# Kernel optimization log

Measured on AMD Instinct MI355X. Metric: run time of the kernel, lower is better.

## Reference

```python
import jax, jax.numpy as jnp
import numpy as np

B, L, D, DK, T = 8192, 64, 512, 64, 128
WIDE_IN = 2 * T + T * T  # 16640


def setup_inputs() -> dict:
    key = jax.random.key(0)
    ks = jax.random.split(key, 24)
    s = 0.02
    inp = {
        "mashup_tags": jax.random.uniform(ks[0], (B, T), jnp.float32),
        "target_api_tags": jax.random.uniform(ks[1], (B, T), jnp.float32),
        "cross_product_tag": jax.random.uniform(ks[2], (B, T * T), jnp.float32),
        "encoded_api_context": jax.random.normal(ks[3], (B, L, D), jnp.float32),
        "candidate_api_description_feature": jax.random.normal(ks[4], (B, D), jnp.float32),
        "mashup_description_feature": jax.random.normal(ks[5], (B, D), jnp.float32),
        "context_len": jax.random.randint(ks[6], (B,), 0, L + 1, jnp.int64 if jax.config.jax_enable_x64 else jnp.int32),
        # attention projections (torch Linear weight layout: [out, in], no bias)
        "W_K": s * jax.random.normal(ks[7], (DK, D), jnp.float32),
        "W_Q": s * jax.random.normal(ks[8], (DK, D), jnp.float32),
        # wide head
        "wide_w": s * jax.random.normal(ks[9], (1, WIDE_IN), jnp.float32),
        "wide_b": jnp.zeros((1,), jnp.float32),
        # deep MLP 1536->512->256->128->1
        "d1_w": s * jax.random.normal(ks[10], (512, 3 * D), jnp.float32),
        "d1_b": jnp.zeros((512,), jnp.float32),
        "d2_w": s * jax.random.normal(ks[11], (256, 512), jnp.float32),
        "d2_b": jnp.zeros((256,), jnp.float32),
        "d3_w": s * jax.random.normal(ks[12], (128, 256), jnp.float32),
        "d3_b": jnp.zeros((128,), jnp.float32),
        "d4_w": s * jax.random.normal(ks[13], (1, 128), jnp.float32),
        "d4_b": jnp.zeros((1,), jnp.float32),
        "wide_weight": jnp.ones((1,), jnp.float32),
        "deep_weight": jnp.ones((1,), jnp.float32),
        "bias": jnp.zeros((1,), jnp.float32),
    }
    return inp


def reference(mashup_tags, target_api_tags, cross_product_tag,
              encoded_api_context, candidate_api_description_feature,
              mashup_description_feature, context_len,
              W_K, W_Q, wide_w, wide_b,
              d1_w, d1_b, d2_w, d2_b, d3_w, d3_b, d4_w, d4_b,
              wide_weight, deep_weight, bias):
    # ---- wide branch ----
    wide_in = jnp.concatenate([mashup_tags, target_api_tags, cross_product_tag], axis=1)
    wide_out = jax.nn.sigmoid(wide_in @ wide_w.T + wide_b)  # (B,1)

    # ---- ragged attention (vectorized masked softmax replaces the Python batch loop) ----
    K = jnp.einsum("bld,kd->blk", encoded_api_context, W_K)          # (B,L,dk)
    Q = candidate_api_description_feature @ W_Q.T                     # (B,dk)
    scores = jnp.einsum("blk,bk->bl", K, Q)                           # (B,L)
    mask = jnp.arange(scores.shape[1])[None, :] < context_len[:, None]
    m = jnp.max(jnp.where(mask, scores, -1e30), axis=-1, keepdims=True)
    e = jnp.where(mask, jnp.exp(scores - m), 0.0)
    denom = jnp.sum(e, axis=-1, keepdims=True)
    probs = e / jnp.maximum(denom, 1e-30)  # rows with length==0 -> all zeros (matches torch zeros fallback)
    api_context = jnp.einsum("bl,bld->bd", probs, encoded_api_context)  # (B,512)

    # ---- deep branch ----
    deep_in = jnp.concatenate([mashup_description_feature, api_context,
                               candidate_api_description_feature], axis=1)  # (B,1536)
    h = jax.nn.relu(deep_in @ d1_w.T + d1_b)
    h = jax.nn.relu(h @ d2_w.T + d2_b)
    h = jax.nn.relu(h @ d3_w.T + d3_b)
    deep_out = h @ d4_w.T + d4_b  # (B,1)

    out = wide_weight * wide_out + deep_weight * deep_out + bias
    return jax.nn.sigmoid(out)
```

## Files before the change

### kernel.cpp

```cpp
#include <hip/hip_runtime.h>

#define Bsz 8192
#define Lctx 64
#define Ddim 512
#define DK 64
#define Ttag 128
#define RQT 4

using f32x4 = __attribute__((ext_vector_type(4))) float;
using bf16x8 = __attribute__((ext_vector_type(8))) short;

__device__ __forceinline__ float wave_sum(float v) {
#pragma unroll
    for (int m = 32; m > 0; m >>= 1) v += __shfl_xor(v, m, 64);
    return v;
}

__device__ __forceinline__ float dot4(float4 a, float4 b) {
    return a.x * b.x + a.y * b.y + a.z * b.z + a.w * b.w;
}

__device__ __forceinline__ unsigned f2bf(float f) {
    unsigned int u = __float_as_uint(f);
    u = u + 0x7fffu + ((u >> 16) & 1u);
    return u >> 16;
}
__device__ __forceinline__ unsigned pack2(float a, float b) {
    return f2bf(a) | (f2bf(b) << 16);
}
__device__ __forceinline__ float bf2f(unsigned short u) { return __uint_as_float((unsigned)u << 16); }

__global__ __launch_bounds__(256) void k_f2bf3(
    const float* __restrict__ s1, unsigned short* __restrict__ d1,
    const float* __restrict__ s2, unsigned short* __restrict__ d2,
    const float* __restrict__ s3, unsigned short* __restrict__ d3)
{
    int i = blockIdx.x * 256 + threadIdx.x;
    const float* s;
    unsigned short* d;
    if (i < 196608)      { s = s1; d = d1; }
    else if (i < 229376) { i -= 196608; s = s2; d = d2; }
    else if (i < 237568) { i -= 229376; s = s3; d = d3; }
    else return;
    const float4 v = ((const float4*)s)[i];
    uint2 w;
    w.x = pack2(v.x, v.y);
    w.y = pack2(v.z, v.w);
    *(uint2*)&d[(size_t)i * 4] = w;
}

__global__ __launch_bounds__(256) void k_qtilde(
    const float* __restrict__ C, const float* __restrict__ WQ,
    const float* __restrict__ WK, float* __restrict__ qt)
{
    const int lane = threadIdx.x & 63;
    const int gw = blockIdx.x * 4 + (threadIdx.x >> 6);
    const int b0 = gw * RQT;

    float4 c0[RQT], c1[RQT];
#pragma unroll
    for (int r = 0; r < RQT; ++r) {
        const float4* row = (const float4*)(C + (size_t)(b0 + r) * Ddim);
        c0[r] = row[lane];
        c1[r] = row[64 + lane];
    }
    float tv[RQT];
#pragma unroll
    for (int r = 0; r < RQT; ++r) tv[r] = 0.f;
    for (int k = 0; k < DK; ++k) {
        const float4* wrow = (const float4*)(WQ + (size_t)k * Ddim);
        const float4 w0 = wrow[lane];
        const float4 w1 = wrow[64 + lane];
#pragma unroll
        for (int r = 0; r < RQT; ++r) {
            float p = dot4(c0[r], w0) + dot4(c1[r], w1);
            p = wave_sum(p);
            if (lane == k) tv[r] = p;
        }
    }
    float4 a0[RQT], a1[RQT];
#pragma unroll
    for (int r = 0; r < RQT; ++r) {
        a0[r] = make_float4(0.f, 0.f, 0.f, 0.f);
        a1[r] = make_float4(0.f, 0.f, 0.f, 0.f);
    }
    for (int k = 0; k < DK; ++k) {
        const float4* wrow = (const float4*)(WK + (size_t)k * Ddim);
        const float4 w0 = wrow[lane];
        const float4 w1 = wrow[64 + lane];
#pragma unroll
        for (int r = 0; r < RQT; ++r) {
            const float tk = __shfl(tv[r], k, 64);
            a0[r].x += tk * w0.x; a0[r].y += tk * w0.y;
            a0[r].z += tk * w0.z; a0[r].w += tk * w0.w;
            a1[r].x += tk * w1.x; a1[r].y += tk * w1.y;
            a1[r].z += tk * w1.z; a1[r].w += tk * w1.w;
        }
    }
#pragma unroll
    for (int r = 0; r < RQT; ++r) {
        float4* orow = (float4*)(qt + (size_t)(b0 + r) * Ddim);
        orow[lane] = a0[r];
        orow[64 + lane] = a1[r];
    }
}

__global__ __launch_bounds__(256, 4) void k_attn_wide(
    const float* __restrict__ X, const float* __restrict__ qt,
    const int* __restrict__ clen, const float* __restrict__ mdesc,
    const float* __restrict__ cand,
    const float* __restrict__ mt, const float* __restrict__ tt,
    const float* __restrict__ cp, const float* __restrict__ ww,
    const float* __restrict__ wb,
    unsigned short* __restrict__ din, float* __restrict__ wl)
{
    const int tid = threadIdx.x;
    const int wave = tid >> 6, lane = tid & 63;
    const int b = blockIdx.x * 4 + wave;
    const int len = clen[b];

    const float4* qrow = (const float4*)(qt + (size_t)b * Ddim);
    const float4 q0 = qrow[lane];
    const float4 q1 = qrow[64 + lane];
    const float4* xb = (const float4*)(X + (size_t)b * Lctx * Ddim);

    float4 y0 = make_float4(0.f, 0.f, 0.f, 0.f);
    float4 y1 = make_float4(0.f, 0.f, 0.f, 0.f);
    float M = -1e30f, D = 0.f;

    const int nch = (len + 7) >> 3;
    for (int c = 0; c < nch; ++c) {
        const int base = c * 8;
        const int nr = min(8, len - base);
        float4 t0[8], t1[8];
#pragma unroll
        for (int r = 0; r < 8; ++r) {
            const int l = base + min(r, nr - 1);
            t0[r] = xb[l * 128 + lane];
            t1[r] = xb[l * 128 + 64 + lane];
        }
        float sc[8];
#pragma unroll
        for (int r = 0; r < 8; ++r)
            sc[r] = dot4(t0[r], q0) + dot4(t1[r], q1);
#pragma unroll
        for (int r = 0; r < 8; ++r) sc[r] = wave_sum(sc[r]);

        float pmax = -1e30f;
#pragma unroll
        for (int r = 0; r < 8; ++r)
            if (r < nr) pmax = fmaxf(pmax, sc[r]);
        const float Mn = fmaxf(M, pmax);
        const float scale = __expf(M - Mn);
        D *= scale;
        y0.x *= scale; y0.y *= scale; y0.z *= scale; y0.w *= scale;
        y1.x *= scale; y1.y *= scale; y1.z *= scale; y1.w *= scale;
#pragma unroll
        for (int r = 0; r < 8; ++r) {
            if (r < nr) {
                const float e = __expf(sc[r] - Mn);
                D += e;
                y0.x += e * t0[r].x; y0.y += e * t0[r].y;
                y0.z += e * t0[r].z; y0.w += e * t0[r].w;
                y1.x += e * t1[r].x; y1.y += e * t1[r].y;
                y1.z += e * t1[r].z; y1.w += e * t1[r].w;
            }
        }
        M = Mn;
    }

    float wacc;
    {
        const float2 a  = ((const float2*)(mt + (size_t)b * Ttag))[lane];
        const float2 wA = ((const float2*)ww)[lane];
        const float2 t  = ((const float2*)(tt + (size_t)b * Ttag))[lane];
        const float2 wB = ((const float2*)(ww + Ttag))[lane];
        wacc = a.x * wA.x + a.y * wA.y + t.x * wB.x + t.y * wB.y;
    }
    {
        const float4* cp4 = (const float4*)(cp + (size_t)b * (Ttag * Ttag));
        const float4* ww4 = (const float4*)(ww + 2 * Ttag);
        float wa = 0.f, wbk = 0.f;
#pragma unroll 8
        for (int i = 0; i < 64; i += 2) {
            wa  += dot4(cp4[i * 64 + lane],       ww4[i * 64 + lane]);
            wbk += dot4(cp4[(i + 1) * 64 + lane], ww4[(i + 1) * 64 + lane]);
        }
        wacc += wa + wbk;
    }
    wacc = wave_sum(wacc);
    if (lane == 0) wl[b] = wacc + wb[0];

    unsigned short* dr = din + (size_t)b * 1536;
    const float rden = 1.f / fmaxf(D, 1e-30f);
    {
        uint2 w;
        w.x = pack2(y0.x * rden, y0.y * rden);
        w.y = pack2(y0.z * rden, y0.w * rden);
        *(uint2*)&dr[512 + 4 * lane] = w;
        w.x = pack2(y1.x * rden, y1.y * rden);
        w.y = pack2(y1.z * rden, y1.w * rden);
        *(uint2*)&dr[512 + 256 + 4 * lane] = w;
    }
    {
        const float4* md = (const float4*)(mdesc + (size_t)b * Ddim);
        const float4 m0 = md[lane], m1 = md[64 + lane];
        uint2 w;
        w.x = pack2(m0.x, m0.y); w.y = pack2(m0.z, m0.w);
        *(uint2*)&dr[4 * lane] = w;
        w.x = pack2(m1.x, m1.y); w.y = pack2(m1.z, m1.w);
        *(uint2*)&dr[256 + 4 * lane] = w;
    }
    {
        const float4* cd = (const float4*)(cand + (size_t)b * Ddim);
        const float4 c0 = cd[lane], c1 = cd[64 + lane];
        uint2 w;
        w.x = pack2(c0.x, c0.y); w.y = pack2(c0.z, c0.w);
        *(uint2*)&dr[1024 + 4 * lane] = w;
        w.x = pack2(c1.x, c1.y); w.y = pack2(c1.z, c1.w);
        *(uint2*)&dr[1024 + 256 + 4 * lane] = w;
    }
}

__global__ __launch_bounds__(256) void k_gemm_bf16(
    const unsigned short* __restrict__ A, const unsigned short* __restrict__ W,
    const float* __restrict__ bias, unsigned short* __restrict__ C,
    const int K, const int N, const int relu)
{
    __shared__ unsigned short As[128][72];
    __shared__ unsigned short Bs[128][72];
    const int tid = threadIdx.x;
    const int wave = tid >> 6, lane = tid & 63;
    const int wm = wave >> 1, wn = wave & 1;
    const size_t m0 = (size_t)blockIdx.x * 128;
    const size_t n0 = (size_t)blockIdx.y * 128;

    f32x4 acc[4][4];
#pragma unroll
    for (int i = 0; i < 4; ++i)
#pragma unroll
        for (int j = 0; j < 4; ++j) acc[i][j] = (f32x4){0.f, 0.f, 0.f, 0.f};

    uint4 pa[4], pb[4];
    auto loadA = [&](int k0) {
#pragma unroll
        for (int j = 0; j < 4; ++j) {
            const int i = tid + j * 256;
            const int row = i >> 3, c8 = (i & 7) * 8;
            pa[j] = *(const uint4*)(A + (m0 + row) * (size_t)K + k0 + c8);
        }
    };
    auto loadB = [&](int k0) {
#pragma unroll
        for (int j = 0; j < 4; ++j) {
            const int i = tid + j * 256;
            const int row = i >> 3, c8 = (i & 7) * 8;
            pb[j] = *(const uint4*)(W + (n0 + row) * (size_t)K + k0 + c8);
        }
    };

    loadA(0);
    loadB(0);
    for (int k0 = 0; k0 < K; k0 += 64) {
        __syncthreads();
#pragma unroll
        for (int j = 0; j < 4; ++j) {
            const int i = tid + j * 256;
            const int row = i >> 3, c8 = (i & 7) * 8;
            *(uint4*)&As[row][c8] = pa[j];
            *(uint4*)&Bs[row][c8] = pb[j];
        }
        __syncthreads();
        if (k0 + 64 < K) { loadA(k0 + 64); loadB(k0 + 64); }
#pragma unroll
        for (int kk = 0; kk < 2; ++kk) {
            const int krow = kk * 32 + (lane >> 4) * 8;
            bf16x8 af[4], bfr[4];
#pragma unroll
            for (int mm = 0; mm < 4; ++mm)
                af[mm] = *(const bf16x8*)&As[wm * 64 + mm * 16 + (lane & 15)][krow];
#pragma unroll
            for (int nn = 0; nn < 4; ++nn)
                bfr[nn] = *(const bf16x8*)&Bs[wn * 64 + nn * 16 + (lane & 15)][krow];
#pragma unroll
            for (int mm = 0; mm < 4; ++mm)
#pragma unroll
                for (int nn = 0; nn < 4; ++nn)
                    acc[mm][nn] = __builtin_amdgcn_mfma_f32_16x16x32_bf16(
                        af[mm], bfr[nn], acc[mm][nn], 0, 0, 0);
        }
    }

#pragma unroll
    for (int nn = 0; nn < 4; ++nn) {
        const int col = (int)n0 + wn * 64 + nn * 16 + (lane & 15);
        const float bv = bias[col];
#pragma unroll
        for (int mm = 0; mm < 4; ++mm) {
#pragma unroll
            for (int r = 0; r < 4; ++r) {
                const size_t row = m0 + wm * 64 + mm * 16 + (lane >> 4) * 4 + r;
                float v = acc[mm][nn][r] + bv;
                if (relu) v = fmaxf(v, 0.f);
                C[row * N + col] = (unsigned short)f2bf(v);
            }
        }
    }
}

__global__ __launch_bounds__(256) void k_final(
    const unsigned short* __restrict__ h3, const float* __restrict__ d4w,
    const float* __restrict__ d4b, const float* __restrict__ wl,
    const float* __restrict__ wwt, const float* __restrict__ dwt,
    const float* __restrict__ bs, float* __restrict__ out)
{
    const int lane = threadIdx.x & 63;
    const int b = blockIdx.x * 4 + (threadIdx.x >> 6);
    const unsigned short* hr = h3 + (size_t)b * 128;
    float v = bf2f(hr[lane]) * d4w[lane] + bf2f(hr[64 + lane]) * d4w[64 + lane];
    v = wave_sum(v);
    if (lane == 0) {
        const float deep = v + d4b[0];
        const float wo = 1.f / (1.f + __expf(-wl[b]));
        const float z = wwt[0] * wo + dwt[0] * deep + bs[0];
        out[b] = 1.f / (1.f + __expf(-z));
    }
}

extern "C" void kernel_launch(void* const* d_in, const int* in_sizes, int n_in,
                              void* d_out, int out_size, void* d_ws, size_t ws_size,
                              hipStream_t stream)
{
    const float* mt    = (const float*)d_in[0];
    const float* tt    = (const float*)d_in[1];
    const float* cp    = (const float*)d_in[2];
    const float* X     = (const float*)d_in[3];
    const float* cand  = (const float*)d_in[4];
    const float* mdesc = (const float*)d_in[5];
    const int*   clen  = (const int*)d_in[6];
    const float* WK    = (const float*)d_in[7];
    const float* WQ    = (const float*)d_in[8];
    const float* ww    = (const float*)d_in[9];
    const float* wb    = (const float*)d_in[10];
    const float* d1w   = (const float*)d_in[11];
    const float* d1b   = (const float*)d_in[12];
    const float* d2w   = (const float*)d_in[13];
    const float* d2b   = (const float*)d_in[14];
    const float* d3w   = (const float*)d_in[15];
    const float* d3b   = (const float*)d_in[16];
    const float* d4w   = (const float*)d_in[17];
    const float* d4b   = (const float*)d_in[18];
    const float* wwt   = (const float*)d_in[19];
    const float* dwt   = (const float*)d_in[20];
    const float* bs    = (const float*)d_in[21];
    float* out = (float*)d_out;

    char* w = (char*)d_ws;
    unsigned short* din = (unsigned short*)w;            w += (size_t)Bsz * 1536 * 2;
    float* qt           = (float*)w;                     w += (size_t)Bsz * 512 * 4;
    unsigned short* h1  = (unsigned short*)w;            w += (size_t)Bsz * 512 * 2;
    unsigned short* h2  = (unsigned short*)w;            w += (size_t)Bsz * 256 * 2;
    unsigned short* h3  = (unsigned short*)w;            w += (size_t)Bsz * 128 * 2;
    float* wl           = (float*)w;                     w += (size_t)Bsz * 4;
    unsigned short* w1b = (unsigned short*)w;            w += (size_t)512 * 1536 * 2;
    unsigned short* w2b = (unsigned short*)w;            w += (size_t)256 * 512 * 2;
    unsigned short* w3b = (unsigned short*)w;            w += (size_t)128 * 256 * 2;

    hipLaunchKernelGGL(k_f2bf3, dim3(928), dim3(256), 0, stream,
                       d1w, w1b, d2w, w2b, d3w, w3b);
    hipLaunchKernelGGL(k_qtilde, dim3(Bsz / (RQT * 4)), dim3(256), 0, stream,
                       cand, WQ, WK, qt);
    hipLaunchKernelGGL(k_attn_wide, dim3(Bsz / 4), dim3(256), 0, stream,
                       X, qt, clen, mdesc, cand, mt, tt, cp, ww, wb, din, wl);
    hipLaunchKernelGGL(k_gemm_bf16, dim3(64, 4), dim3(256), 0, stream,
                       din, w1b, d1b, h1, 1536, 512, 1);
    hipLaunchKernelGGL(k_gemm_bf16, dim3(64, 2), dim3(256), 0, stream,
                       h1, w2b, d2b, h2, 512, 256, 1);
    hipLaunchKernelGGL(k_gemm_bf16, dim3(64, 1), dim3(256), 0, stream,
                       h2, w3b, d3b, h3, 256, 128, 1);
    hipLaunchKernelGGL(k_final, dim3(Bsz / 4), dim3(256), 0, stream,
                       h3, d4w, d4b, wl, wwt, dwt, bs, out);
}
```

Measured before the change: 438.5 us.

## Split wide head into per-row kernel and use narrower GEMM tiles

Moves the wide-branch dot product out of the attention kernel into a separate kernel with one 256-thread block per batch row. The attention chunk size drops from 8 to 4 context rows, and the bf16 GEMM is templated on N-tile width, using 64-wide tiles to double the grid size for the MLP layers. The goal is more memory-level parallelism and better CU occupancy. The cost is an extra launch, less load batching in attention, and more A-tile reloads in the GEMM.

Result: no change. 440.7 us (+0.5%).

```diff
diff --git a/kernel.cpp b/kernel.cpp
--- a/kernel.cpp
+++ b/kernel.cpp
@@ -105,14 +105,10 @@
     }
 }
 
-__global__ __launch_bounds__(256, 4) void k_attn_wide(
+__global__ __launch_bounds__(256, 4) void k_attn(
     const float* __restrict__ X, const float* __restrict__ qt,
     const int* __restrict__ clen, const float* __restrict__ mdesc,
-    const float* __restrict__ cand,
-    const float* __restrict__ mt, const float* __restrict__ tt,
-    const float* __restrict__ cp, const float* __restrict__ ww,
-    const float* __restrict__ wb,
-    unsigned short* __restrict__ din, float* __restrict__ wl)
+    const float* __restrict__ cand, unsigned short* __restrict__ din)
 {
     const int tid = threadIdx.x;
     const int wave = tid >> 6, lane = tid & 63;
@@ -128,27 +124,27 @@
     float4 y1 = make_float4(0.f, 0.f, 0.f, 0.f);
     float M = -1e30f, D = 0.f;
 
-    const int nch = (len + 7) >> 3;
+    const int nch = (len + 3) >> 2;
     for (int c = 0; c < nch; ++c) {
-        const int base = c * 8;
-        const int nr = min(8, len - base);
-        float4 t0[8], t1[8];
-#pragma unroll
-        for (int r = 0; r < 8; ++r) {
+        const int base = c * 4;
+        const int nr = min(4, len - base);
+        float4 t0[4], t1[4];
+#pragma unroll
+        for (int r = 0; r < 4; ++r) {
             const int l = base + min(r, nr - 1);
             t0[r] = xb[l * 128 + lane];
             t1[r] = xb[l * 128 + 64 + lane];
         }
-        float sc[8];
-#pragma unroll
-        for (int r = 0; r < 8; ++r)
+        float sc[4];
+#pragma unroll
+        for (int r = 0; r < 4; ++r)
             sc[r] = dot4(t0[r], q0) + dot4(t1[r], q1);
 #pragma unroll
-        for (int r = 0; r < 8; ++r) sc[r] = wave_sum(sc[r]);
+        for (int r = 0; r < 4; ++r) sc[r] = wave_sum(sc[r]);
 
         float pmax = -1e30f;
 #pragma unroll
-        for (int r = 0; r < 8; ++r)
+        for (int r = 0; r < 4; ++r)
             if (r < nr) pmax = fmaxf(pmax, sc[r]);
         const float Mn = fmaxf(M, pmax);
         const float scale = __expf(M - Mn);
@@ -156,7 +152,7 @@
         y0.x *= scale; y0.y *= scale; y0.z *= scale; y0.w *= scale;
         y1.x *= scale; y1.y *= scale; y1.z *= scale; y1.w *= scale;
 #pragma unroll
-        for (int r = 0; r < 8; ++r) {
+        for (int r = 0; r < 4; ++r) {
             if (r < nr) {
                 const float e = __expf(sc[r] - Mn);
                 D += e;
@@ -168,28 +164,6 @@
         }
         M = Mn;
     }
-
-    float wacc;
-    {
-        const float2 a  = ((const float2*)(mt + (size_t)b * Ttag))[lane];
-        const float2 wA = ((const float2*)ww)[lane];
-        const float2 t  = ((const float2*)(tt + (size_t)b * Ttag))[lane];
-        const float2 wB = ((const float2*)(ww + Ttag))[lane];
-        wacc = a.x * wA.x + a.y * wA.y + t.x * wB.x + t.y * wB.y;
-    }
-    {
-        const float4* cp4 = (const float4*)(cp + (size_t)b * (Ttag * Ttag));
-        const float4* ww4 = (const float4*)(ww + 2 * Ttag);
-        float wa = 0.f, wbk = 0.f;
-#pragma unroll 8
-        for (int i = 0; i < 64; i += 2) {
-            wa  += dot4(cp4[i * 64 + lane],       ww4[i * 64 + lane]);
-            wbk += dot4(cp4[(i + 1) * 64 + lane], ww4[(i + 1) * 64 + lane]);
-        }
-        wacc += wa + wbk;
-    }
-    wacc = wave_sum(wacc);
-    if (lane == 0) wl[b] = wacc + wb[0];
 
     unsigned short* dr = din + (size_t)b * 1536;
     const float rden = 1.f / fmaxf(D, 1e-30f);
@@ -222,26 +196,57 @@
     }
 }
 
+__global__ __launch_bounds__(256) void k_wide(
+    const float* __restrict__ mt, const float* __restrict__ tt,
+    const float* __restrict__ cp, const float* __restrict__ ww,
+    const float* __restrict__ wb, float* __restrict__ wl)
+{
+    const int b = blockIdx.x;
+    const int tid = threadIdx.x;
+    const int wave = tid >> 6, lane = tid & 63;
+    float acc = 0.f;
+    if (tid < 64) {
+        float4 v;
+        if (tid < 32) v = ((const float4*)(mt + (size_t)b * Ttag))[tid];
+        else          v = ((const float4*)(tt + (size_t)b * Ttag))[tid - 32];
+        acc += dot4(v, ((const float4*)ww)[tid]);
+    }
+    const float4* cp4 = (const float4*)(cp + (size_t)b * (Ttag * Ttag));
+    const float4* ww4 = (const float4*)(ww + 2 * Ttag);
+#pragma unroll 4
+    for (int i = tid; i < (Ttag * Ttag) / 4; i += 256)
+        acc += dot4(cp4[i], ww4[i]);
+    acc = wave_sum(acc);
+    __shared__ float red[4];
+    if (lane == 0) red[wave] = acc;
+    __syncthreads();
+    if (tid == 0) wl[b] = red[0] + red[1] + red[2] + red[3] + wb[0];
+}
+
+template <int BN>
 __global__ __launch_bounds__(256) void k_gemm_bf16(
     const unsigned short* __restrict__ A, const unsigned short* __restrict__ W,
     const float* __restrict__ bias, unsigned short* __restrict__ C,
     const int K, const int N, const int relu)
 {
+    constexpr int WN = BN / 2;
+    constexpr int NN = WN / 16;
+    constexpr int NB = (BN * 8) / 256;
     __shared__ unsigned short As[128][72];
-    __shared__ unsigned short Bs[128][72];
+    __shared__ unsigned short Bs[BN][72];
     const int tid = threadIdx.x;
     const int wave = tid >> 6, lane = tid & 63;
     const int wm = wave >> 1, wn = wave & 1;
     const size_t m0 = (size_t)blockIdx.x * 128;
-    const size_t n0 = (size_t)blockIdx.y * 128;
-
-    f32x4 acc[4][4];
+    const size_t n0 = (size_t)blockIdx.y * BN;
+
+    f32x4 acc[4][NN];
 #pragma unroll
     for (int i = 0; i < 4; ++i)
 #pragma unroll
-        for (int j = 0; j < 4; ++j) acc[i][j] = (f32x4){0.f, 0.f, 0.f, 0.f};
-
-    uint4 pa[4], pb[4];
+        for (int j = 0; j < NN; ++j) acc[i][j] = (f32x4){0.f, 0.f, 0.f, 0.f};
+
+    uint4 pa[4], pb[NB];
     auto loadA = [&](int k0) {
 #pragma unroll
         for (int j = 0; j < 4; ++j) {
@@ -252,7 +257,7 @@
     };
     auto loadB = [&](int k0) {
 #pragma unroll
-        for (int j = 0; j < 4; ++j) {
+        for (int j = 0; j < NB; ++j) {
             const int i = tid + j * 256;
             const int row = i >> 3, c8 = (i & 7) * 8;
             pb[j] = *(const uint4*)(W + (n0 + row) * (size_t)K + k0 + c8);
@@ -268,6 +273,11 @@
             const int i = tid + j * 256;
             const int row = i >> 3, c8 = (i & 7) * 8;
             *(uint4*)&As[row][c8] = pa[j];
+        }
+#pragma unroll
+        for (int j = 0; j < NB; ++j) {
+            const int i = tid + j * 256;
+            const int row = i >> 3, c8 = (i & 7) * 8;
             *(uint4*)&Bs[row][c8] = pb[j];
         }
         __syncthreads();
@@ -275,25 +285,25 @@
 #pragma unroll
         for (int kk = 0; kk < 2; ++kk) {
             const int krow = kk * 32 + (lane >> 4) * 8;
-            bf16x8 af[4], bfr[4];
+            bf16x8 af[4], bfr[NN];
 #pragma unroll
             for (int mm = 0; mm < 4; ++mm)
                 af[mm] = *(const bf16x8*)&As[wm * 64 + mm * 16 + (lane & 15)][krow];
 #pragma unroll
-            for (int nn = 0; nn < 4; ++nn)
-                bfr[nn] = *(const bf16x8*)&Bs[wn * 64 + nn * 16 + (lane & 15)][krow];
+            for (int nn = 0; nn < NN; ++nn)
+                bfr[nn] = *(const bf16x8*)&Bs[wn * WN + nn * 16 + (lane & 15)][krow];
 #pragma unroll
             for (int mm = 0; mm < 4; ++mm)
 #pragma unroll
-                for (int nn = 0; nn < 4; ++nn)
+                for (int nn = 0; nn < NN; ++nn)
                     acc[mm][nn] = __builtin_amdgcn_mfma_f32_16x16x32_bf16(
                         af[mm], bfr[nn], acc[mm][nn], 0, 0, 0);
         }
     }
 
 #pragma unroll
-    for (int nn = 0; nn < 4; ++nn) {
-        const int col = (int)n0 + wn * 64 + nn * 16 + (lane & 15);
+    for (int nn = 0; nn < NN; ++nn) {
+        const int col = (int)n0 + wn * WN + nn * 16 + (lane & 15);
         const float bv = bias[col];
 #pragma unroll
         for (int mm = 0; mm < 4; ++mm) {
@@ -370,13 +380,15 @@
                        d1w, w1b, d2w, w2b, d3w, w3b);
     hipLaunchKernelGGL(k_qtilde, dim3(Bsz / (RQT * 4)), dim3(256), 0, stream,
                        cand, WQ, WK, qt);
-    hipLaunchKernelGGL(k_attn_wide, dim3(Bsz / 4), dim3(256), 0, stream,
-                       X, qt, clen, mdesc, cand, mt, tt, cp, ww, wb, din, wl);
-    hipLaunchKernelGGL(k_gemm_bf16, dim3(64, 4), dim3(256), 0, stream,
+    hipLaunchKernelGGL(k_attn, dim3(Bsz / 4), dim3(256), 0, stream,
+                       X, qt, clen, mdesc, cand, din);
+    hipLaunchKernelGGL(k_wide, dim3(Bsz), dim3(256), 0, stream,
+                       mt, tt, cp, ww, wb, wl);
+    hipLaunchKernelGGL((k_gemm_bf16<64>), dim3(64, 8), dim3(256), 0, stream,
                        din, w1b, d1b, h1, 1536, 512, 1);
-    hipLaunchKernelGGL(k_gemm_bf16, dim3(64, 2), dim3(256), 0, stream,
+    hipLaunchKernelGGL((k_gemm_bf16<64>), dim3(64, 4), dim3(256), 0, stream,
                        h1, w2b, d2b, h2, 512, 256, 1);
-    hipLaunchKernelGGL(k_gemm_bf16, dim3(64, 1), dim3(256), 0, stream,
+    hipLaunchKernelGGL((k_gemm_bf16<64>), dim3(64, 2), dim3(256), 0, stream,
                        h2, w3b, d3b, h3, 256, 128, 1);
     hipLaunchKernelGGL(k_final, dim3(Bsz / 4), dim3(256), 0, stream,
                        h3, d4w, d4b, wl, wwt, dwt, bs, out);
```
